# Kernel optimization log

Hardware: AMD Instinct MI355X
Metric: run time of the kernel (lower is better)

Reference implementation:

```python
import jax, jax.numpy as jnp
import numpy as np

# Dims from init_kwargs
B, L, D = 32, 512, 1024
NSEC = 4
SSIZE = D // NSEC          # 256
LATENT = 256
N_TOKENS = 32
BANDS = ((0, 64), (16, 128), (32, 192), (64, 256))
COEF = 0.1


def _dct_mat(N):
    # torch_dct.dct (DCT-II, unnormalized, factor 2): X[k] = 2*sum_n x[n] cos(pi*k*(2n+1)/(2N))
    n = jnp.arange(N, dtype=jnp.float32)
    k = jnp.arange(N, dtype=jnp.float32)[:, None]
    return 2.0 * jnp.cos(jnp.pi * (2.0 * n + 1.0) * k / (2.0 * N))  # [k, n]


def _idct_mat(N):
    # exact inverse of the above (DCT-III form): x[n] = (1/N)*(X[0]/2 + sum_{k>=1} X[k] cos(pi*k*(2n+1)/(2N)))
    k = jnp.arange(N, dtype=jnp.float32)
    n = jnp.arange(N, dtype=jnp.float32)[:, None]
    M = jnp.cos(jnp.pi * k * (2.0 * n + 1.0) / (2.0 * N)) / N
    return M.at[:, 0].set(1.0 / (2.0 * N))  # [n, k]


def setup_inputs() -> dict:
    key = jax.random.key(0)
    k1, k2, k3 = jax.random.split(key, 3)
    encoding = jax.random.normal(k1, (B, L, D), dtype=jnp.float32)
    W = jax.random.normal(k2, (LATENT, SSIZE), dtype=jnp.float32) / np.float32(np.sqrt(SSIZE))
    b = jax.random.normal(k3, (LATENT,), dtype=jnp.float32) * 0.01
    return {"encoding": encoding, "W": W, "b": b}


def reference(encoding, W, b):
    # encoding: [B, L, D] -> [B, L, NSEC, SSIZE]
    enc = encoding.reshape(B, L, NSEC, SSIZE)
    # Literal semantics of the torch code: H = enc[:,:,i] is [B,L,S]; H.T -> [S,L,B];
    # dct/idct act over the LAST axis (= batch), scaling indexes the seq axis.
    C = _dct_mat(B)   # [k, b]
    M = _idct_mat(B)  # [b, k]
    # DCT along batch axis for all sectors at once: [k, L, NSEC, SSIZE]
    Dk = jnp.einsum('kb,blns->klns', C, enc)
    # Per-sector band scaling along the seq axis
    seq = jnp.arange(L)
    mask = jnp.stack(
        [jnp.where((seq < lo) | (seq >= hi), jnp.float32(COEF), jnp.float32(1.0)) for (lo, hi) in BANDS],
        axis=1,
    )  # [L, NSEC]
    Dk = Dk * mask[None, :, :, None]
    # IDCT back along batch axis: [B, L, NSEC, SSIZE]
    filt = jnp.einsum('bk,klns->blns', M, Dk)
    # Linear(SSIZE -> LATENT) + tanh, then keep first N_TOKENS positions
    y = jnp.tanh(jnp.einsum('blns,os->blno', filt, W) + b)
    return y[:, :N_TOKENS]
```

## Files before the change

### kernel.cpp

```cpp
#include <hip/hip_runtime.h>
#include <math.h>

#define BATCH    32
#define LSEQ     512
#define DDIM     1024
#define SSIZE    256
#define LATENT   256
#define COEF     0.1f

#define ROWS     4096
#define COLS     256
#define KDIM     256

#define TR   32
#define TC   64
#define STR  260


__device__ __forceinline__ float tanh_fast(float x) {
    return 1.0f - 2.0f / (__expf(2.0f * x) + 1.0f);
}

__global__ __launch_bounds__(256, 8)
void transpose_w_kernel(const float* __restrict__ W, float* __restrict__ Wt) {
    __shared__ float tile[32][33];
    const int tx = threadIdx.x;
    const int ty = threadIdx.y;
    const int bx = blockIdx.x;
    const int by = blockIdx.y;
    #pragma unroll
    for (int i = 0; i < 4; ++i) {
        const int o = by * 32 + ty + i * 8;
        const int k = bx * 32 + tx;
        tile[ty + i * 8][tx] = W[o * KDIM + k];
    }
    __syncthreads();
    #pragma unroll
    for (int i = 0; i < 4; ++i) {
        const int k = bx * 32 + ty + i * 8;
        const int o = by * 32 + tx;
        Wt[k * COLS + o] = tile[tx][ty + i * 8];
    }
}

__global__ __launch_bounds__(256, 2)
void spectral_gemm_kernel(const float* __restrict__ enc,
                          const float* __restrict__ Wt,
                          const float* __restrict__ bias,
                          float* __restrict__ out) {
    __shared__ float As[TR * STR];

    const int t      = threadIdx.x;
    const int tile_r = blockIdx.x * TR;
    const int tile_c = blockIdx.y * TC;

    const float* src = enc + (long)(tile_r >> 7) * (long)(LSEQ * DDIM)
                           + (long)(tile_r & 127) * 256;
    #pragma unroll
    for (int it = 0; it < 8; ++it) {
        const int f = t + it * 256;
        const int r = f >> 6;
        const int k = (f & 63) << 2;
        const float4 v = *(const float4*)(src + (long)f * 4);
        *(float4*)&As[r * STR + k] = v;
    }
    __syncthreads();

    const int ty = t >> 4;
    const int tx = t & 15;
    const int r0 = 2 * ty;
    const float* wp = Wt + tile_c + tx * 4;

    float acc0x = 0.f, acc0y = 0.f, acc0z = 0.f, acc0w = 0.f;
    float acc1x = 0.f, acc1y = 0.f, acc1z = 0.f, acc1w = 0.f;

    #pragma unroll 4
    for (int k = 0; k < KDIM; k += 4) {
        const float4 a0 = *(const float4*)&As[r0 * STR + k];
        const float4 a1 = *(const float4*)&As[(r0 + 1) * STR + k];
        const float4 w0 = *(const float4*)(wp + (long)(k + 0) * COLS);
        const float4 w1 = *(const float4*)(wp + (long)(k + 1) * COLS);
        const float4 w2 = *(const float4*)(wp + (long)(k + 2) * COLS);
        const float4 w3 = *(const float4*)(wp + (long)(k + 3) * COLS);

        acc0x += a0.x * w0.x; acc0y += a0.x * w0.y; acc0z += a0.x * w0.z; acc0w += a0.x * w0.w;
        acc0x += a0.y * w1.x; acc0y += a0.y * w1.y; acc0z += a0.y * w1.z; acc0w += a0.y * w1.w;
        acc0x += a0.z * w2.x; acc0y += a0.z * w2.y; acc0z += a0.z * w2.z; acc0w += a0.z * w2.w;
        acc0x += a0.w * w3.x; acc0y += a0.w * w3.y; acc0z += a0.w * w3.z; acc0w += a0.w * w3.w;

        acc1x += a1.x * w0.x; acc1y += a1.x * w0.y; acc1z += a1.x * w0.z; acc1w += a1.x * w0.w;
        acc1x += a1.y * w1.x; acc1y += a1.y * w1.y; acc1z += a1.y * w1.z; acc1w += a1.y * w1.w;
        acc1x += a1.z * w2.x; acc1y += a1.z * w2.y; acc1z += a1.z * w2.z; acc1w += a1.z * w2.w;
        acc1x += a1.w * w3.x; acc1y += a1.w * w3.y; acc1z += a1.w * w3.z; acc1w += a1.w * w3.w;
    }

    const float4 b4 = *(const float4*)&bias[tile_c + tx * 4];
    float accs[2][4] = {{acc0x, acc0y, acc0z, acc0w}, {acc1x, acc1y, acc1z, acc1w}};
    #pragma unroll
    for (int i = 0; i < 2; ++i) {
        const int row = tile_r + r0 + i;
        const int n = row & 3;
        const int l = (row >> 2) & 31;
        const float scale = (n == 0 || (n == 1 && l >= 16)) ? 1.0f : COEF;
        float4 o;
        o.x = tanh_fast(scale * accs[i][0] + b4.x);
        o.y = tanh_fast(scale * accs[i][1] + b4.y);
        o.z = tanh_fast(scale * accs[i][2] + b4.z);
        o.w = tanh_fast(scale * accs[i][3] + b4.w);
        *(float4*)&out[(long)row * COLS + tile_c + tx * 4] = o;
    }
}

extern "C" void kernel_launch(void* const* d_in, const int* in_sizes, int n_in,
                              void* d_out, int out_size, void* d_ws, size_t ws_size,
                              hipStream_t stream) {
    const float* enc  = (const float*)d_in[0];
    const float* W    = (const float*)d_in[1];
    const float* bias = (const float*)d_in[2];
    float* out = (float*)d_out;
    float* Wt  = (float*)d_ws;

    transpose_w_kernel<<<dim3(8, 8), dim3(32, 8), 0, stream>>>(W, Wt);

    dim3 grid(ROWS / TR, COLS / TC);
    spectral_gemm_kernel<<<grid, dim3(256), 0, stream>>>(enc, Wt, bias, out);
}
```

Baseline: 111.2 us.

## Drop W transpose kernel and stage W tiles in shared memory per K-chunk

```diff
diff --git a/kernel.cpp b/kernel.cpp
--- a/kernel.cpp
+++ b/kernel.cpp
@@ -1,113 +1,100 @@
 #include <hip/hip_runtime.h>
 #include <math.h>
 
-#define BATCH    32
-#define LSEQ     512
-#define DDIM     1024
-#define SSIZE    256
-#define LATENT   256
-#define COEF     0.1f
+#define LSEQ   512
+#define DDIM   1024
+#define KDIM   256
+#define COLS   256
+#define ROWS   4096
+#define COEF   0.1f
 
-#define ROWS     4096
-#define COLS     256
-#define KDIM     256
-
-#define TR   32
-#define TC   64
-#define STR  260
+#define TR    32
+#define TC    64
+#define BK    64
+#define STRA  260
+#define STRW  68
 
 
 __device__ __forceinline__ float tanh_fast(float x) {
     return 1.0f - 2.0f / (__expf(2.0f * x) + 1.0f);
 }
 
-__global__ __launch_bounds__(256, 8)
-void transpose_w_kernel(const float* __restrict__ W, float* __restrict__ Wt) {
-    __shared__ float tile[32][33];
-    const int tx = threadIdx.x;
-    const int ty = threadIdx.y;
-    const int bx = blockIdx.x;
-    const int by = blockIdx.y;
-    #pragma unroll
-    for (int i = 0; i < 4; ++i) {
-        const int o = by * 32 + ty + i * 8;
-        const int k = bx * 32 + tx;
-        tile[ty + i * 8][tx] = W[o * KDIM + k];
-    }
-    __syncthreads();
-    #pragma unroll
-    for (int i = 0; i < 4; ++i) {
-        const int k = bx * 32 + ty + i * 8;
-        const int o = by * 32 + tx;
-        Wt[k * COLS + o] = tile[tx][ty + i * 8];
-    }
-}
-
 __global__ __launch_bounds__(256, 2)
 void spectral_gemm_kernel(const float* __restrict__ enc,
-                          const float* __restrict__ Wt,
+                          const float* __restrict__ W,
                           const float* __restrict__ bias,
                           float* __restrict__ out) {
-    __shared__ float As[TR * STR];
+    __shared__ float As[TR * STRA];
+    __shared__ float Ws[TC * STRW];
 
     const int t      = threadIdx.x;
     const int tile_r = blockIdx.x * TR;
     const int tile_c = blockIdx.y * TC;
 
-    const float* src = enc + (long)(tile_r >> 7) * (long)(LSEQ * DDIM)
-                           + (long)(tile_r & 127) * 256;
+    const float* srcA = enc + (size_t)(tile_r >> 7) * (size_t)(LSEQ * DDIM)
+                            + (size_t)(tile_r & 127) * KDIM;
     #pragma unroll
     for (int it = 0; it < 8; ++it) {
-        const int f = t + it * 256;
-        const int r = f >> 6;
-        const int k = (f & 63) << 2;
-        const float4 v = *(const float4*)(src + (long)f * 4);
-        *(float4*)&As[r * STR + k] = v;
-    }
-    __syncthreads();
-
-    const int ty = t >> 4;
-    const int tx = t & 15;
-    const int r0 = 2 * ty;
-    const float* wp = Wt + tile_c + tx * 4;
-
-    float acc0x = 0.f, acc0y = 0.f, acc0z = 0.f, acc0w = 0.f;
-    float acc1x = 0.f, acc1y = 0.f, acc1z = 0.f, acc1w = 0.f;
-
-    #pragma unroll 4
-    for (int k = 0; k < KDIM; k += 4) {
-        const float4 a0 = *(const float4*)&As[r0 * STR + k];
-        const float4 a1 = *(const float4*)&As[(r0 + 1) * STR + k];
-        const float4 w0 = *(const float4*)(wp + (long)(k + 0) * COLS);
-        const float4 w1 = *(const float4*)(wp + (long)(k + 1) * COLS);
-        const float4 w2 = *(const float4*)(wp + (long)(k + 2) * COLS);
-        const float4 w3 = *(const float4*)(wp + (long)(k + 3) * COLS);
-
-        acc0x += a0.x * w0.x; acc0y += a0.x * w0.y; acc0z += a0.x * w0.z; acc0w += a0.x * w0.w;
-        acc0x += a0.y * w1.x; acc0y += a0.y * w1.y; acc0z += a0.y * w1.z; acc0w += a0.y * w1.w;
-        acc0x += a0.z * w2.x; acc0y += a0.z * w2.y; acc0z += a0.z * w2.z; acc0w += a0.z * w2.w;
-        acc0x += a0.w * w3.x; acc0y += a0.w * w3.y; acc0z += a0.w * w3.z; acc0w += a0.w * w3.w;
-
-        acc1x += a1.x * w0.x; acc1y += a1.x * w0.y; acc1z += a1.x * w0.z; acc1w += a1.x * w0.w;
-        acc1x += a1.y * w1.x; acc1y += a1.y * w1.y; acc1z += a1.y * w1.z; acc1w += a1.y * w1.w;
-        acc1x += a1.z * w2.x; acc1y += a1.z * w2.y; acc1z += a1.z * w2.z; acc1w += a1.z * w2.w;
-        acc1x += a1.w * w3.x; acc1y += a1.w * w3.y; acc1z += a1.w * w3.z; acc1w += a1.w * w3.w;
+        const int f  = t + it * 256;
+        const int r  = f >> 6;
+        const int k4 = f & 63;
+        const float4 v = *(const float4*)(srcA + (size_t)f * 4);
+        *(float4*)&As[r * STRA + k4 * 4] = v;
     }
 
-    const float4 b4 = *(const float4*)&bias[tile_c + tx * 4];
-    float accs[2][4] = {{acc0x, acc0y, acc0z, acc0w}, {acc1x, acc1y, acc1z, acc1w}};
+    const int tx = t & 15;
+    const int ty = t >> 4;
+    const int r0 = 2 * ty;
+
+    float acc[2][4] = {{0.f,0.f,0.f,0.f},{0.f,0.f,0.f,0.f}};
+
+    for (int p = 0; p < 4; ++p) {
+        const int kk = p * BK;
+
+        #pragma unroll
+        for (int it = 0; it < 4; ++it) {
+            const int o  = (t >> 4) + it * 16;
+            const int k4 = t & 15;
+            const float4 v =
+                *(const float4*)&W[(size_t)(tile_c + o) * KDIM + kk + k4 * 4];
+            *(float4*)&Ws[o * STRW + k4 * 4] = v;
+        }
+        __syncthreads();
+
+        #pragma unroll 8
+        for (int k = 0; k < BK; k += 4) {
+            const float4 a0 = *(const float4*)&As[r0 * STRA + kk + k];
+            const float4 a1 = *(const float4*)&As[(r0 + 1) * STRA + kk + k];
+            float4 w[4];
+            #pragma unroll
+            for (int c = 0; c < 4; ++c)
+                w[c] = *(const float4*)&Ws[(tx + 16 * c) * STRW + k];
+            #pragma unroll
+            for (int c = 0; c < 4; ++c) {
+                acc[0][c] += a0.x * w[c].x;
+                acc[0][c] += a0.y * w[c].y;
+                acc[0][c] += a0.z * w[c].z;
+                acc[0][c] += a0.w * w[c].w;
+                acc[1][c] += a1.x * w[c].x;
+                acc[1][c] += a1.y * w[c].y;
+                acc[1][c] += a1.z * w[c].z;
+                acc[1][c] += a1.w * w[c].w;
+            }
+        }
+        __syncthreads();
+    }
+
     #pragma unroll
     for (int i = 0; i < 2; ++i) {
         const int row = tile_r + r0 + i;
         const int n = row & 3;
         const int l = (row >> 2) & 31;
         const float scale = (n == 0 || (n == 1 && l >= 16)) ? 1.0f : COEF;
-        float4 o;
-        o.x = tanh_fast(scale * accs[i][0] + b4.x);
-        o.y = tanh_fast(scale * accs[i][1] + b4.y);
-        o.z = tanh_fast(scale * accs[i][2] + b4.z);
-        o.w = tanh_fast(scale * accs[i][3] + b4.w);
-        *(float4*)&out[(long)row * COLS + tile_c + tx * 4] = o;
+        #pragma unroll
+        for (int c = 0; c < 4; ++c) {
+            const int col = tile_c + tx + 16 * c;
+            out[(size_t)row * COLS + col] = tanh_fast(scale * acc[i][c] + bias[col]);
+        }
     }
 }
 
@@ -118,10 +105,7 @@
     const float* W    = (const float*)d_in[1];
     const float* bias = (const float*)d_in[2];
     float* out = (float*)d_out;
-    float* Wt  = (float*)d_ws;
-
-    transpose_w_kernel<<<dim3(8, 8), dim3(32, 8), 0, stream>>>(W, Wt);
 
     dim3 grid(ROWS / TR, COLS / TC);
-    spectral_gemm_kernel<<<grid, dim3(256), 0, stream>>>(enc, Wt, bias, out);
+    spectral_gemm_kernel<<<grid, dim3(256), 0, stream>>>(enc, W, bias, out);
 }
```

Result: faster. 102.9 us (-7.5%).
